# Kernel tuning notes

Hardware: AMD Instinct MI355X
Metric: run time of the kernel (lower is better)

The kernel has to match this reference:

```python
import jax, jax.numpy as jnp
from jax import lax
import numpy as np

M_BITS = 10      # retained mantissa bits (fp32 has 23)
BLOCK_K = 128    # accumulation block size along K


def round_mantissa(x, m_bits=M_BITS):
    """Round-to-nearest-even the fp32 mantissa to m_bits via bit manipulation.
    Exponent carry on mantissa overflow is handled naturally by integer add."""
    if m_bits >= 23:
        return x
    shift = 23 - m_bits
    b = lax.bitcast_convert_type(x, jnp.int32)
    # round-half-to-even bias: (lsb_kept) + (2^(shift-1) - 1)
    rb = ((b >> shift) & 1) + ((1 << (shift - 1)) - 1)
    b = (b + rb) & ~((1 << shift) - 1)
    return lax.bitcast_convert_type(b, jnp.float32)


def setup_inputs() -> dict:
    key = jax.random.key(0)
    k1, k2, k3 = jax.random.split(key, 3)
    M, K, N = 8192, 4096, 4096
    x = jax.random.normal(k1, (M, K), dtype=jnp.float32)
    weight = jax.random.normal(k2, (N, K), dtype=jnp.float32)  # [out, in] like torch Linear
    bias = jax.random.normal(k3, (N,), dtype=jnp.float32)
    return {"x": x, "weight": weight, "bias": bias}


def reference(x, weight, bias):
    # out = custom_accum_gemm(x, weight.T): blockwise K accumulation with
    # mantissa rounding applied to the accumulator after every block.
    M, K = x.shape
    N = weight.shape[0]
    nblk = K // BLOCK_K
    xb = x.reshape(M, nblk, BLOCK_K).transpose(1, 0, 2)        # [nblk, M, bk]
    wb = weight.T.reshape(nblk, BLOCK_K, N)                    # [nblk, bk, N]

    def step(acc, blk):
        xk, wk = blk
        acc = round_mantissa(acc + xk @ wk)
        return acc, None

    acc0 = jnp.zeros((M, N), dtype=jnp.float32)
    out, _ = lax.scan(step, acc0, (xb, wb))
    # bias add followed by mantissa rounding (as in forward)
    return round_mantissa(out + bias)
```

## Files before the change

kernel.cpp:

```cpp
#include <hip/hip_runtime.h>
#include <stdint.h>
#include <stddef.h>

typedef __attribute__((ext_vector_type(4))) float f32x4;
typedef __attribute__((ext_vector_type(8))) short bf16x8;

#define BMN 256
#define BK  64
#define NTHREADS 512

__device__ __forceinline__ float round_m10(float x) {
    int b = __float_as_int(x);
    int rb = ((b >> 13) & 1) + 0x0FFF;
    b = (b + rb) & (int)0xFFFFE000;
    return __int_as_float(b);
}

__device__ __forceinline__ unsigned short f32_to_bf16(float x) {
    unsigned int u = __float_as_uint(x);
    u += 0x7FFFu + ((u >> 16) & 1u);
    return (unsigned short)(u >> 16);
}

__global__ void convert2_f32_bf16_swz(const float* __restrict__ inx,
                                      unsigned short* __restrict__ outx,
                                      const float* __restrict__ inw,
                                      unsigned short* __restrict__ outw,
                                      long nx8, long ntot, int cpr) {
    long g = (long)blockIdx.x * blockDim.x + threadIdx.x;
    const long stride = (long)gridDim.x * blockDim.x;
    for (; g < ntot; g += stride) {
        const float* in;
        unsigned short* out;
        long gg;
        if (g < nx8) { in = inx; out = outx; gg = g; }
        else         { in = inw; out = outw; gg = g - nx8; }
        const long row = gg / cpr;
        const int c = (int)(gg - row * cpr);
        const float* p = in + gg * 8;
        f32x4 v0 = *(const f32x4*)p;
        f32x4 v1 = *(const f32x4*)(p + 4);
        bf16x8 o;
        o[0] = (short)f32_to_bf16(v0[0]); o[1] = (short)f32_to_bf16(v0[1]);
        o[2] = (short)f32_to_bf16(v0[2]); o[3] = (short)f32_to_bf16(v0[3]);
        o[4] = (short)f32_to_bf16(v1[0]); o[5] = (short)f32_to_bf16(v1[1]);
        o[6] = (short)f32_to_bf16(v1[2]); o[7] = (short)f32_to_bf16(v1[3]);
        const int cdst = (c & ~7) | ((c & 7) ^ ((int)row & 7));
        *(bf16x8*)(out + (row * (long)cpr + cdst) * 8) = o;
    }
}

__device__ __forceinline__ void gload_lds16(const unsigned short* g, unsigned short* l) {
    __builtin_amdgcn_global_load_lds(
        (const __attribute__((address_space(1))) void*)g,
        (__attribute__((address_space(3))) void*)l, 16, 0, 0);
}

__device__ __forceinline__ void stage_half(const unsigned short* __restrict__ G,
                                           unsigned short* lds,
                                           int grow0, int gcol, int K, int tid) {
    const int wave = tid >> 6;
#pragma unroll
    for (int p = 0; p < 2; ++p) {
        const int s = tid + p * NTHREADS;
        const int row = s >> 3;
        const unsigned short* g = G + (size_t)(grow0 + row) * K + gcol + (s & 7) * 8;
        unsigned short* l = lds + (size_t)(wave * 64 + p * NTHREADS) * 8;
        gload_lds16(g, l);
    }
}

__global__ __launch_bounds__(NTHREADS, 2)
void gemm8p(const unsigned short* __restrict__ Abf, const unsigned short* __restrict__ Bbf,
            const float* __restrict__ bias, float* __restrict__ out,
            int M, int N, int K) {
    __shared__ unsigned short sA[2][2][128 * 64];
    __shared__ unsigned short sB[2][2][128 * 64];

    const int tid  = threadIdx.x;
    const int lane = tid & 63;
    const int wave = tid >> 6;
    const int wm = wave >> 2;
    const int wn = wave & 3;
    const int lrow = lane & 15;
    const int lkg  = lane >> 4;
    const int NT = K / BK;

    const int gx = gridDim.x;
    const int nwg = gx * gridDim.y;
    int lin = blockIdx.y * gx + blockIdx.x;
    if ((nwg & 7) == 0) lin = (lin & 7) * (nwg >> 3) + (lin >> 3);
    const int bm0 = (lin / gx) * BMN;
    const int bn0 = (lin % gx) * BMN;

    const int r7   = lrow & 7;
    const int lco0 = (lkg ^ r7) * 8;
    const int lco1 = lco0 ^ 32;
    const int Aoff0 = lrow * 64 + lco0;
    const int Aoff1 = lrow * 64 + lco1;
    const int Boff0 = ((wn & 1) * 64 + lrow) * 64 + lco0;
    const int Boff1 = ((wn & 1) * 64 + lrow) * 64 + lco1;

    const unsigned short* Ab0 = &sA[0][wm][0];
    const unsigned short* Ab1 = &sA[1][wm][0];
    const unsigned short* Bb0 = &sB[0][wn >> 1][0];
    const unsigned short* Bb1 = &sB[1][wn >> 1][0];

    f32x4 acc[8][4];
    const f32x4 zero = {0.f, 0.f, 0.f, 0.f};
#pragma unroll
    for (int i = 0; i < 8; ++i)
#pragma unroll
        for (int j = 0; j < 4; ++j) acc[i][j] = zero;

    bf16x8 aS0[4], aS1[4], bS0[4], bS1[4];

#define RD_A(dst, base, q, off) { const unsigned short* _pa = (base); \
    _Pragma("unroll") for (int i = 0; i < 4; ++i) \
        dst[i] = *(const bf16x8*)&_pa[((q) * 4 + i) * 1024 + (off)]; }
#define RD_B(dst, base, off) { const unsigned short* _pb = (base); \
    _Pragma("unroll") for (int j = 0; j < 4; ++j) \
        dst[j] = *(const bf16x8*)&_pb[j * 1024 + (off)]; }

#define PH(q, aU, bU, RDS, STG, VMW) \
    STG \
    VMW \
    __builtin_amdgcn_s_barrier(); \
    asm volatile("s_waitcnt lgkmcnt(0)"); \
    __builtin_amdgcn_sched_barrier(0); \
    __builtin_amdgcn_s_setprio(1); \
    _Pragma("unroll") for (int i = 0; i < 4; ++i) \
    _Pragma("unroll") for (int j = 0; j < 4; ++j) \
        acc[(q) * 4 + i][j] = __builtin_amdgcn_mfma_f32_16x16x32_bf16(aU[i], bU[j], acc[(q) * 4 + i][j], 0, 0, 0); \
    __builtin_amdgcn_s_setprio(0); \
    RDS

    stage_half(Abf, &sA[0][0][0], bm0,       0,  K, tid);
    stage_half(Abf, &sA[0][1][0], bm0 + 128, 0,  K, tid);
    stage_half(Bbf, &sB[0][0][0], bn0,       0,  K, tid);
    stage_half(Bbf, &sB[0][1][0], bn0 + 128, 0,  K, tid);
    stage_half(Bbf, &sB[1][0][0], bn0,       BK, K, tid);
    stage_half(Bbf, &sB[1][1][0], bn0 + 128, BK, K, tid);
    asm volatile("s_waitcnt vmcnt(4)");
    __builtin_amdgcn_s_barrier();
    RD_A(aS0, Ab0, 0, Aoff0)
    RD_B(bS0, Bb0, Boff0)

    for (int t = 0; t < NT; t += 2) {
        int u2 = t + 2; if (u2 >= NT) u2 -= NT;
        int u3 = t + 3; if (u3 >= NT) u3 -= NT;
        const int k1 = (t + 1) * BK, k2 = u2 * BK, k3 = u3 * BK;

        PH(0, aS0, bS0,
           RD_A(aS1, Ab0, 1, Aoff0),
           stage_half(Abf, &sA[1][0][0], bm0, k1, K, tid);, )

        PH(1, aS1, bS0,
           RD_A(aS0, Ab0, 0, Aoff1) RD_B(bS1, Bb0, Boff1),
           stage_half(Abf, &sA[1][1][0], bm0 + 128, k1, K, tid);, )

        PH(0, aS0, bS1,
           RD_A(aS1, Ab0, 1, Aoff1), , )

        PH(1, aS1, bS1,
           RD_A(aS0, Ab1, 0, Aoff0) RD_B(bS0, Bb1, Boff0),
           stage_half(Bbf, &sB[0][0][0], bn0, k2, K, tid);,
           asm volatile("s_waitcnt vmcnt(2)");)

        PH(0, aS0, bS0,
           RD_A(aS1, Ab1, 1, Aoff0),
           stage_half(Bbf, &sB[0][1][0], bn0 + 128, k2, K, tid);, )

        PH(1, aS1, bS0,
           RD_A(aS0, Ab1, 0, Aoff1) RD_B(bS1, Bb1, Boff1),
           stage_half(Abf, &sA[0][0][0], bm0, k2, K, tid);, )

        PH(0, aS0, bS1,
           RD_A(aS1, Ab1, 1, Aoff1),
           stage_half(Abf, &sA[0][1][0], bm0 + 128, k2, K, tid);, )

        PH(1, aS1, bS1,
           RD_A(aS0, Ab0, 0, Aoff0) RD_B(bS0, Bb0, Boff0),
           stage_half(Bbf, &sB[1][0][0], bn0, k3, K, tid);
           stage_half(Bbf, &sB[1][1][0], bn0 + 128, k3, K, tid);,
           asm volatile("s_waitcnt vmcnt(4)");)
    }

    asm volatile("s_waitcnt vmcnt(0) lgkmcnt(0)" ::: "memory");

#pragma unroll
    for (int ia = 0; ia < 8; ++ia) {
        const int row = bm0 + wm * 128 + ia * 16 + lkg * 4;
#pragma unroll
        for (int j = 0; j < 4; ++j) {
            const int col = bn0 + wn * 64 + j * 16 + lrow;
            const float bv = bias[col];
#pragma unroll
            for (int r = 0; r < 4; ++r)
                out[(size_t)(row + r) * N + col] = round_m10(acc[ia][j][r] + bv);
        }
    }
#undef RD_A
#undef RD_B
#undef PH
}

__global__ __launch_bounds__(256)
void gemm_fallback(const float* __restrict__ A, const float* __restrict__ B,
                   const float* __restrict__ bias, float* __restrict__ out,
                   int M, int N, int K) {
    __shared__ unsigned short lds_a[128 * 64];
    __shared__ unsigned short lds_b[128 * 64];
    const int tid = threadIdx.x, lane = tid & 63, wave = tid >> 6;
    const int wm = wave >> 1, wn = wave & 1;
    const int bm0 = blockIdx.y * 128, bn0 = blockIdx.x * 128;
    const int lrow = lane & 15, lkg = lane >> 4;
    f32x4 acc[4][4];
    const f32x4 zero = {0.f, 0.f, 0.f, 0.f};
#pragma unroll
    for (int i = 0; i < 4; ++i)
#pragma unroll
        for (int j = 0; j < 4; ++j) acc[i][j] = zero;
    for (int kb = 0; kb < K / 64; ++kb) {
        const int kt = kb * 64;
        const int r0 = tid >> 4, c0 = (tid & 15) << 2;
#pragma unroll
        for (int p = 0; p < 8; ++p) {
            const int r = p * 16 + r0;
            f32x4 va = *(const f32x4*)(A + (size_t)(bm0 + r) * K + kt + c0);
            f32x4 vb = *(const f32x4*)(B + (size_t)(bn0 + r) * K + kt + c0);
            ushort4 ua, ub;
            ua.x = f32_to_bf16(va[0]); ua.y = f32_to_bf16(va[1]);
            ua.z = f32_to_bf16(va[2]); ua.w = f32_to_bf16(va[3]);
            ub.x = f32_to_bf16(vb[0]); ub.y = f32_to_bf16(vb[1]);
            ub.z = f32_to_bf16(vb[2]); ub.w = f32_to_bf16(vb[3]);
            *(ushort4*)(&lds_a[r * 64 + c0]) = ua;
            *(ushort4*)(&lds_b[r * 64 + c0]) = ub;
        }
        __syncthreads();
#pragma unroll
        for (int kk = 0; kk < 64; kk += 32) {
            bf16x8 af[4], bfr[4];
#pragma unroll
            for (int i = 0; i < 4; ++i)
                af[i] = *(const bf16x8*)(&lds_a[(wm * 64 + i * 16 + lrow) * 64 + kk + lkg * 8]);
#pragma unroll
            for (int j = 0; j < 4; ++j)
                bfr[j] = *(const bf16x8*)(&lds_b[(wn * 64 + j * 16 + lrow) * 64 + kk + lkg * 8]);
#pragma unroll
            for (int i = 0; i < 4; ++i)
#pragma unroll
                for (int j = 0; j < 4; ++j)
                    acc[i][j] = __builtin_amdgcn_mfma_f32_16x16x32_bf16(af[i], bfr[j], acc[i][j], 0, 0, 0);
        }
        __syncthreads();
    }
#pragma unroll
    for (int i = 0; i < 4; ++i) {
        const int row0 = bm0 + wm * 64 + i * 16 + lkg * 4;
#pragma unroll
        for (int j = 0; j < 4; ++j) {
            const int col = bn0 + wn * 64 + j * 16 + lrow;
            const float bv = bias[col];
#pragma unroll
            for (int r = 0; r < 4; ++r)
                out[(size_t)(row0 + r) * N + col] = round_m10(acc[i][j][r] + bv);
        }
    }
}

extern "C" void kernel_launch(void* const* d_in, const int* in_sizes, int n_in,
                              void* d_out, int out_size, void* d_ws, size_t ws_size,
                              hipStream_t stream) {
    const float* x    = (const float*)d_in[0];
    const float* w    = (const float*)d_in[1];
    const float* bias = (const float*)d_in[2];
    float* out = (float*)d_out;

    const int N = in_sizes[2];
    const int K = in_sizes[1] / N;
    const int M = in_sizes[0] / K;

    const size_t nx = (size_t)M * K;
    const size_t nw = (size_t)N * K;
    const size_t need = (nx + nw) * sizeof(unsigned short);
    const int NT = K / BK;

    if (ws_size >= need && (M % BMN) == 0 && (N % BMN) == 0 && (K % BK) == 0 &&
        NT >= 4 && (NT % 2) == 0) {
        unsigned short* xb = (unsigned short*)d_ws;
        unsigned short* wb = xb + nx;
        const int cpr = K / 8;
        convert2_f32_bf16_swz<<<2048, 256, 0, stream>>>(
            x, xb, w, wb, (long)(nx / 8), (long)((nx + nw) / 8), cpr);
        dim3 grid(N / BMN, M / BMN);
        gemm8p<<<grid, NTHREADS, 0, stream>>>(xb, wb, bias, out, M, N, K);
    } else {
        dim3 grid(N / 128, M / 128);
        gemm_fallback<<<grid, 256, 0, stream>>>(x, w, bias, out, M, N, K);
    }
}
```

Before: 271.4 us.

## Replace register double-buffered fragment pipeline with single-buffer reads and simpler staging

The fragment registers drop from double buffers (aS0/aS1, bS0/bS1) to single av/bv arrays, and the LDS reads move to the start of each phase instead of overlapping the previous phase's MFMAs. Global staging now stages A and B together for the next K tile with full vmcnt(0) waits, and an extra barrier is added after each MFMA phase. This lowers register pressure and simplifies the schedule, but the LDS-read latency is no longer hidden behind MFMA work and the added barriers cost extra synchronisation.

```diff
diff --git a/kernel.cpp b/kernel.cpp
--- a/kernel.cpp
+++ b/kernel.cpp
@@ -113,16 +113,17 @@
 #pragma unroll
         for (int j = 0; j < 4; ++j) acc[i][j] = zero;
 
-    bf16x8 aS0[4], aS1[4], bS0[4], bS1[4];
-
-#define RD_A(dst, base, q, off) { const unsigned short* _pa = (base); \
+    bf16x8 av[4], bv[4];
+
+#define RD_A(base, q, off) { const unsigned short* _pa = (base); \
     _Pragma("unroll") for (int i = 0; i < 4; ++i) \
-        dst[i] = *(const bf16x8*)&_pa[((q) * 4 + i) * 1024 + (off)]; }
-#define RD_B(dst, base, off) { const unsigned short* _pb = (base); \
+        av[i] = *(const bf16x8*)&_pa[((q) * 4 + i) * 1024 + (off)]; }
+#define RD_B(base, off) { const unsigned short* _pb = (base); \
     _Pragma("unroll") for (int j = 0; j < 4; ++j) \
-        dst[j] = *(const bf16x8*)&_pb[j * 1024 + (off)]; }
-
-#define PH(q, aU, bU, RDS, STG, VMW) \
+        bv[j] = *(const bf16x8*)&_pb[j * 1024 + (off)]; }
+
+#define PH(q, RDS, STG, VMW) \
+    RDS \
     STG \
     VMW \
     __builtin_amdgcn_s_barrier(); \
@@ -131,59 +132,48 @@
     __builtin_amdgcn_s_setprio(1); \
     _Pragma("unroll") for (int i = 0; i < 4; ++i) \
     _Pragma("unroll") for (int j = 0; j < 4; ++j) \
-        acc[(q) * 4 + i][j] = __builtin_amdgcn_mfma_f32_16x16x32_bf16(aU[i], bU[j], acc[(q) * 4 + i][j], 0, 0, 0); \
+        acc[(q) * 4 + i][j] = __builtin_amdgcn_mfma_f32_16x16x32_bf16(av[i], bv[j], acc[(q) * 4 + i][j], 0, 0, 0); \
     __builtin_amdgcn_s_setprio(0); \
-    RDS
-
-    stage_half(Abf, &sA[0][0][0], bm0,       0,  K, tid);
-    stage_half(Abf, &sA[0][1][0], bm0 + 128, 0,  K, tid);
-    stage_half(Bbf, &sB[0][0][0], bn0,       0,  K, tid);
-    stage_half(Bbf, &sB[0][1][0], bn0 + 128, 0,  K, tid);
-    stage_half(Bbf, &sB[1][0][0], bn0,       BK, K, tid);
-    stage_half(Bbf, &sB[1][1][0], bn0 + 128, BK, K, tid);
-    asm volatile("s_waitcnt vmcnt(4)");
+    __builtin_amdgcn_s_barrier(); \
+    __builtin_amdgcn_sched_barrier(0);
+
+    stage_half(Abf, &sA[0][0][0], bm0,       0, K, tid);
+    stage_half(Abf, &sA[0][1][0], bm0 + 128, 0, K, tid);
+    stage_half(Bbf, &sB[0][0][0], bn0,       0, K, tid);
+    stage_half(Bbf, &sB[0][1][0], bn0 + 128, 0, K, tid);
+    asm volatile("s_waitcnt vmcnt(0)");
     __builtin_amdgcn_s_barrier();
-    RD_A(aS0, Ab0, 0, Aoff0)
-    RD_B(bS0, Bb0, Boff0)
+    __builtin_amdgcn_sched_barrier(0);
 
     for (int t = 0; t < NT; t += 2) {
         int u2 = t + 2; if (u2 >= NT) u2 -= NT;
-        int u3 = t + 3; if (u3 >= NT) u3 -= NT;
-        const int k1 = (t + 1) * BK, k2 = u2 * BK, k3 = u3 * BK;
-
-        PH(0, aS0, bS0,
-           RD_A(aS1, Ab0, 1, Aoff0),
-           stage_half(Abf, &sA[1][0][0], bm0, k1, K, tid);, )
-
-        PH(1, aS1, bS0,
-           RD_A(aS0, Ab0, 0, Aoff1) RD_B(bS1, Bb0, Boff1),
-           stage_half(Abf, &sA[1][1][0], bm0 + 128, k1, K, tid);, )
-
-        PH(0, aS0, bS1,
-           RD_A(aS1, Ab0, 1, Aoff1), , )
-
-        PH(1, aS1, bS1,
-           RD_A(aS0, Ab1, 0, Aoff0) RD_B(bS0, Bb1, Boff0),
-           stage_half(Bbf, &sB[0][0][0], bn0, k2, K, tid);,
-           asm volatile("s_waitcnt vmcnt(2)");)
-
-        PH(0, aS0, bS0,
-           RD_A(aS1, Ab1, 1, Aoff0),
+        const int k1 = (t + 1) * BK, k2 = u2 * BK;
+
+        PH(0, RD_A(Ab0, 0, Aoff0) RD_B(Bb0, Boff0),
+           stage_half(Abf, &sA[1][0][0], bm0, k1, K, tid);
+           stage_half(Bbf, &sB[1][0][0], bn0, k1, K, tid);, )
+
+        PH(1, RD_A(Ab0, 1, Aoff0),
+           stage_half(Abf, &sA[1][1][0], bm0 + 128, k1, K, tid);
+           stage_half(Bbf, &sB[1][1][0], bn0 + 128, k1, K, tid);, )
+
+        PH(0, RD_A(Ab0, 0, Aoff1) RD_B(Bb0, Boff1), , )
+
+        PH(1, RD_A(Ab0, 1, Aoff1), ,
+           asm volatile("s_waitcnt vmcnt(0)");)
+
+        PH(0, RD_A(Ab1, 0, Aoff0) RD_B(Bb1, Boff0),
+           stage_half(Abf, &sA[0][0][0], bm0, k2, K, tid);
+           stage_half(Bbf, &sB[0][0][0], bn0, k2, K, tid);, )
+
+        PH(1, RD_A(Ab1, 1, Aoff0),
+           stage_half(Abf, &sA[0][1][0], bm0 + 128, k2, K, tid);
            stage_half(Bbf, &sB[0][1][0], bn0 + 128, k2, K, tid);, )
 
-        PH(1, aS1, bS0,
-           RD_A(aS0, Ab1, 0, Aoff1) RD_B(bS1, Bb1, Boff1),
-           stage_half(Abf, &sA[0][0][0], bm0, k2, K, tid);, )
-
-        PH(0, aS0, bS1,
-           RD_A(aS1, Ab1, 1, Aoff1),
-           stage_half(Abf, &sA[0][1][0], bm0 + 128, k2, K, tid);, )
-
-        PH(1, aS1, bS1,
-           RD_A(aS0, Ab0, 0, Aoff0) RD_B(bS0, Bb0, Boff0),
-           stage_half(Bbf, &sB[1][0][0], bn0, k3, K, tid);
-           stage_half(Bbf, &sB[1][1][0], bn0 + 128, k3, K, tid);,
-           asm volatile("s_waitcnt vmcnt(4)");)
+        PH(0, RD_A(Ab1, 0, Aoff1) RD_B(Bb1, Boff1), , )
+
+        PH(1, RD_A(Ab1, 1, Aoff1), ,
+           asm volatile("s_waitcnt vmcnt(0)");)
     }
 
     asm volatile("s_waitcnt vmcnt(0) lgkmcnt(0)" ::: "memory");
```

New measurement: 304.6 us. +12.2%, slower.

## Restructure GEMM main loop pipeline with deeper LDS read prefetch and partial lgkmcnt waits

Applied to the files above, without the earlier changes.

Reorganizes the software-pipelined bf16 MFMA main loop so both A halves and both B halves of the next K tile are staged together, and the register fragments for the next phase are prefetched two phases ahead instead of one. The per-phase wait changes from draining all LDS reads to partial lgkmcnt counts (4 or 8), and the global-load waits become vmcnt(0) at two points per iteration. The goal is more overlap between LDS reads, global staging and MFMA issue. In exchange it holds more fragment registers live and depends on the LDS-read counts matching the chosen waitcnt values for correctness.

```diff
diff --git a/kernel.cpp b/kernel.cpp
--- a/kernel.cpp
+++ b/kernel.cpp
@@ -122,11 +122,11 @@
     _Pragma("unroll") for (int j = 0; j < 4; ++j) \
         dst[j] = *(const bf16x8*)&_pb[j * 1024 + (off)]; }
 
-#define PH(q, aU, bU, RDS, STG, VMW) \
+#define PH(q, LG, aU, bU, RDS, STG, VMW) \
     STG \
     VMW \
     __builtin_amdgcn_s_barrier(); \
-    asm volatile("s_waitcnt lgkmcnt(0)"); \
+    asm volatile("s_waitcnt lgkmcnt(" LG ")"); \
     __builtin_amdgcn_sched_barrier(0); \
     __builtin_amdgcn_s_setprio(1); \
     _Pragma("unroll") for (int i = 0; i < 4; ++i) \
@@ -139,51 +139,54 @@
     stage_half(Abf, &sA[0][1][0], bm0 + 128, 0,  K, tid);
     stage_half(Bbf, &sB[0][0][0], bn0,       0,  K, tid);
     stage_half(Bbf, &sB[0][1][0], bn0 + 128, 0,  K, tid);
+    stage_half(Abf, &sA[1][0][0], bm0,       BK, K, tid);
+    stage_half(Abf, &sA[1][1][0], bm0 + 128, BK, K, tid);
     stage_half(Bbf, &sB[1][0][0], bn0,       BK, K, tid);
     stage_half(Bbf, &sB[1][1][0], bn0 + 128, BK, K, tid);
-    asm volatile("s_waitcnt vmcnt(4)");
+    asm volatile("s_waitcnt vmcnt(8)");
     __builtin_amdgcn_s_barrier();
     RD_A(aS0, Ab0, 0, Aoff0)
     RD_B(bS0, Bb0, Boff0)
+    RD_A(aS1, Ab0, 1, Aoff0)
 
     for (int t = 0; t < NT; t += 2) {
         int u2 = t + 2; if (u2 >= NT) u2 -= NT;
         int u3 = t + 3; if (u3 >= NT) u3 -= NT;
-        const int k1 = (t + 1) * BK, k2 = u2 * BK, k3 = u3 * BK;
-
-        PH(0, aS0, bS0,
+        const int k2 = u2 * BK, k3 = u3 * BK;
+
+        PH(0, "4", aS0, bS0,
+           RD_A(aS0, Ab0, 0, Aoff1) RD_B(bS1, Bb0, Boff1), , )
+
+        PH(1, "8", aS1, bS0,
+           RD_A(aS1, Ab0, 1, Aoff1), , )
+
+        PH(0, "4", aS0, bS1,
+           RD_A(aS0, Ab1, 0, Aoff0) RD_B(bS0, Bb1, Boff0),
+           , asm volatile("s_waitcnt vmcnt(0)");)
+
+        PH(1, "8", aS1, bS1,
+           RD_A(aS1, Ab1, 1, Aoff0),
+           stage_half(Abf, &sA[0][0][0], bm0, k2, K, tid);
+           stage_half(Bbf, &sB[0][0][0], bn0, k2, K, tid);, )
+
+        PH(0, "4", aS0, bS0,
+           RD_A(aS0, Ab1, 0, Aoff1) RD_B(bS1, Bb1, Boff1),
+           stage_half(Abf, &sA[0][1][0], bm0 + 128, k2, K, tid);
+           stage_half(Bbf, &sB[0][1][0], bn0 + 128, k2, K, tid);, )
+
+        PH(1, "8", aS1, bS0,
+           RD_A(aS1, Ab1, 1, Aoff1), , )
+
+        PH(0, "4", aS0, bS1,
+           RD_A(aS0, Ab0, 0, Aoff0) RD_B(bS0, Bb0, Boff0),
+           , asm volatile("s_waitcnt vmcnt(0)");)
+
+        PH(1, "8", aS1, bS1,
            RD_A(aS1, Ab0, 1, Aoff0),
-           stage_half(Abf, &sA[1][0][0], bm0, k1, K, tid);, )
-
-        PH(1, aS1, bS0,
-           RD_A(aS0, Ab0, 0, Aoff1) RD_B(bS1, Bb0, Boff1),
-           stage_half(Abf, &sA[1][1][0], bm0 + 128, k1, K, tid);, )
-
-        PH(0, aS0, bS1,
-           RD_A(aS1, Ab0, 1, Aoff1), , )
-
-        PH(1, aS1, bS1,
-           RD_A(aS0, Ab1, 0, Aoff0) RD_B(bS0, Bb1, Boff0),
-           stage_half(Bbf, &sB[0][0][0], bn0, k2, K, tid);,
-           asm volatile("s_waitcnt vmcnt(2)");)
-
-        PH(0, aS0, bS0,
-           RD_A(aS1, Ab1, 1, Aoff0),
-           stage_half(Bbf, &sB[0][1][0], bn0 + 128, k2, K, tid);, )
-
-        PH(1, aS1, bS0,
-           RD_A(aS0, Ab1, 0, Aoff1) RD_B(bS1, Bb1, Boff1),
-           stage_half(Abf, &sA[0][0][0], bm0, k2, K, tid);, )
-
-        PH(0, aS0, bS1,
-           RD_A(aS1, Ab1, 1, Aoff1),
-           stage_half(Abf, &sA[0][1][0], bm0 + 128, k2, K, tid);, )
-
-        PH(1, aS1, bS1,
-           RD_A(aS0, Ab0, 0, Aoff0) RD_B(bS0, Bb0, Boff0),
+           stage_half(Abf, &sA[1][0][0], bm0, k3, K, tid);
+           stage_half(Abf, &sA[1][1][0], bm0 + 128, k3, K, tid);
            stage_half(Bbf, &sB[1][0][0], bn0, k3, K, tid);
-           stage_half(Bbf, &sB[1][1][0], bn0 + 128, k3, K, tid);,
-           asm volatile("s_waitcnt vmcnt(4)");)
+           stage_half(Bbf, &sB[1][1][0], bn0 + 128, k3, K, tid);, )
     }
 
     asm volatile("s_waitcnt vmcnt(0) lgkmcnt(0)" ::: "memory");
```

Measured after the change: 293.7 us. 1.08x slower.
